# Kernel tuning notes

Measured on AMD Instinct MI355X. Metric: run time of the kernel, lower is better.

## Reference

```python
import jax, jax.numpy as jnp
import numpy as np

B_SZ, L, D_MODEL = 2, 2048, 2048
D_SSM, D_STATE, NHEADS, HEADDIM = 4096, 128, 64, 64
D_CONV, CHUNK = 3, 128
EPS = 1e-5


def setup_inputs() -> dict:
    key = jax.random.key(0)
    k = jax.random.split(key, 8)
    d_in_proj = 2 * D_SSM + 2 * D_STATE + NHEADS  # 8512
    conv_dim = D_SSM + 2 * D_STATE                # 4352
    # dt_bias init exactly as in the torch module (inverse-softplus of dt)
    dt = jnp.exp(jax.random.uniform(k[5], (NHEADS,)) * (np.log(0.1) - np.log(0.001)) + np.log(0.001))
    dt = jnp.clip(dt, 1e-4, None)
    dt_bias = dt + jnp.log(-jnp.expm1(-dt))
    return {
        "u": jax.random.normal(k[0], (B_SZ, L, D_MODEL), jnp.float32),
        "W_in": jax.random.normal(k[1], (d_in_proj, D_MODEL), jnp.float32) * (D_MODEL ** -0.5),
        "conv_w": jax.random.normal(k[2], (conv_dim, D_CONV), jnp.float32) * (D_CONV ** -0.5),
        "conv_b": jnp.zeros((conv_dim,), jnp.float32),
        "dt_bias": dt_bias,
        "A_log": jnp.log(jax.random.uniform(k[3], (NHEADS,), minval=1.0, maxval=16.0)),
        "D": jnp.ones((NHEADS,), jnp.float32),
        "norm_w": jnp.ones((D_SSM,), jnp.float32),
        "W_out": jax.random.normal(k[4], (D_MODEL, D_SSM), jnp.float32) * (D_SSM ** -0.5),
    }


def _silu(x):
    return x * jax.nn.sigmoid(x)


def _segsum(x):
    # x: (..., T) -> (..., T, T) lower-triangular cumulative segment sums; -inf above diag
    T = x.shape[-1]
    cs = jnp.cumsum(x, axis=-1)
    d = cs[..., :, None] - cs[..., None, :]
    mask = jnp.tril(jnp.ones((T, T), dtype=bool))
    return jnp.where(mask, d, -jnp.inf)


def _ssd(X, A, Bm, Cm):
    # Chunked selective-scan (SSD). X (b,l,h,p) is x*dt; A (b,l,h) is dt*A_head (log-decay);
    # Bm, Cm (b,l,n) with ngroups=1.
    nc = L // CHUNK
    X = X.reshape(B_SZ, nc, CHUNK, NHEADS, HEADDIM)
    A = A.reshape(B_SZ, nc, CHUNK, NHEADS).transpose(0, 3, 1, 2)  # (b,h,c,l)
    Bm = Bm.reshape(B_SZ, nc, CHUNK, D_STATE)
    Cm = Cm.reshape(B_SZ, nc, CHUNK, D_STATE)
    A_cum = jnp.cumsum(A, axis=-1)
    Ld = jnp.exp(_segsum(A))  # (b,h,c,l,s) intra-chunk causal decay
    Y_diag = jnp.einsum('bcln,bcsn,bhcls,bcshp->bclhp', Cm, Bm, Ld, X)
    decay_states = jnp.exp(A_cum[..., -1:] - A_cum)  # (b,h,c,l)
    states = jnp.einsum('bcln,bhcl,bclhp->bchpn', Bm, decay_states, X)
    states = jnp.concatenate([jnp.zeros_like(states[:, :1]), states], axis=1)
    decay_chunk = jnp.exp(_segsum(jnp.pad(A_cum[..., -1], ((0, 0), (0, 0), (1, 0)))))  # (b,h,c+1,c+1)
    states = jnp.einsum('bhzc,bchpn->bzhpn', decay_chunk, states)[:, :-1]  # state entering each chunk
    Y_off = jnp.einsum('bcln,bchpn,bhcl->bclhp', Cm, states, jnp.exp(A_cum))
    return (Y_diag + Y_off).reshape(B_SZ, L, NHEADS, HEADDIM)


def reference(u, W_in, conv_w, conv_b, dt_bias, A_log, D, norm_w, W_out):
    zxbcdt = jnp.einsum('bld,ed->ble', u, W_in)  # in_proj (no bias)
    z = zxbcdt[..., :D_SSM]
    xBC = zxbcdt[..., D_SSM:2 * D_SSM + 2 * D_STATE]
    dt = jax.nn.softplus(zxbcdt[..., -NHEADS:] + dt_bias)  # (b,l,h)
    # causal depthwise conv1d + SiLU
    xpad = jnp.pad(xBC, ((0, 0), (D_CONV - 1, 0), (0, 0)))
    xBC = _silu(sum(xpad[:, k:k + L, :] * conv_w[:, k] for k in range(D_CONV)) + conv_b)
    x = xBC[..., :D_SSM].reshape(B_SZ, L, NHEADS, HEADDIM)
    Bm = xBC[..., D_SSM:D_SSM + D_STATE]
    Cm = xBC[..., D_SSM + D_STATE:]
    A = -jnp.exp(A_log)  # (h,)
    y = _ssd(x * dt[..., None], dt * A, Bm, Cm) + D[None, None, :, None] * x
    # gated RMSNorm (norm_before_gate=False: gate first, then normalize)
    y = y.reshape(B_SZ, L, D_SSM) * _silu(z)
    y = y * jax.lax.rsqrt(jnp.mean(y * y, axis=-1, keepdims=True) + EPS) * norm_w
    out = jnp.einsum('ble,de->bld', y, W_out)  # out_proj (no bias)
    return out + out[:, ::-1, :]  # bimamba v0: out + out.flip(seq)
```

## Files before the change

kernel.cpp:

```cpp
#include <hip/hip_runtime.h>

constexpr int B_SZ = 2, LSEQ = 2048, D_MODEL = 2048;
constexpr int D_SSM = 4096, D_STATE = 128, NHEADS = 64, HEADDIM = 64;
constexpr int CHUNK = 128;
constexpr int NCH = LSEQ / CHUNK;
constexpr int BL = B_SZ * LSEQ;
constexpr int DIN = 2 * D_SSM + 2 * D_STATE + NHEADS;
constexpr int DINP = 8576;
constexpr int CONVDIM = D_SSM + 2 * D_STATE;
constexpr int BOFF = D_SSM;
constexpr int COFF = D_SSM + D_STATE;

constexpr size_t OFF_WIN = 0;
constexpr size_t OFF_UB  = OFF_WIN + (size_t)DINP * D_MODEL * 2;
constexpr size_t OFF_ZX  = OFF_UB + (size_t)BL * D_MODEL * 2;
constexpr size_t OFF_XBC = OFF_ZX + (size_t)BL * DINP * 2;
constexpr size_t OFF_DT  = OFF_XBC + (size_t)BL * CONVDIM * 2;
constexpr size_t OFF_ST  = OFF_DT + (size_t)BL * NHEADS * 4;
constexpr size_t OFF_CB  = OFF_ST + (size_t)B_SZ * NCH * NHEADS * HEADDIM * D_STATE * 4;
constexpr size_t OFF_DAS = OFF_CB + (size_t)B_SZ * NCH * CHUNK * CHUNK * 4;
constexpr size_t WS_NEED = OFF_DAS + (size_t)B_SZ * NCH * NHEADS * 4 + 4096;

typedef float f32x4 __attribute__((ext_vector_type(4)));
typedef __bf16 bf16x8 __attribute__((ext_vector_type(8)));

__device__ __forceinline__ unsigned short f2bf(float f) {
  unsigned int x = __float_as_uint(f);
  x += 0x7fffu + ((x >> 16) & 1u);
  return (unsigned short)(x >> 16);
}
__device__ __forceinline__ float bf2f(unsigned short u) {
  return __uint_as_float(((unsigned int)u) << 16);
}

__device__ __forceinline__ void llds16(const unsigned short* g, unsigned short* l) {
  __builtin_amdgcn_global_load_lds(
      (const __attribute__((address_space(1))) unsigned int*)g,
      (__attribute__((address_space(3))) unsigned int*)l, 16, 0, 0);
}

__global__ void k_cvt4(const float4* __restrict__ src, ushort4* __restrict__ dst,
                       int n4, int nsrc4) {
  int i = blockIdx.x * 256 + threadIdx.x;
  if (i >= n4) return;
  float4 v = make_float4(0.f, 0.f, 0.f, 0.f);
  if (i < nsrc4) v = src[i];
  ushort4 o;
  o.x = f2bf(v.x); o.y = f2bf(v.y); o.z = f2bf(v.z); o.w = f2bf(v.w);
  dst[i] = o;
}

template <bool OUT_BF16>
__global__ __launch_bounds__(256, 2) void k_gemm_bt(
    const unsigned short* __restrict__ A, const unsigned short* __restrict__ Bm,
    void* __restrict__ Cv, int M, int N, int K) {
  __shared__ __align__(16) unsigned short As[128 * 32];
  __shared__ __align__(16) unsigned short Bs[128 * 32];
  int t = threadIdx.x;
  int mt = M >> 7, ntl = N >> 7;
  int bid = blockIdx.x;
  int panel = bid / (8 * mt);
  int within = bid - panel * 8 * mt;
  int pw = min(8, ntl - panel * 8);
  int m0 = (within / pw) * 128;
  int n0 = (panel * 8 + within % pw) * 128;
  int w = t >> 6, lane = t & 63;
  int wm = (w >> 1) * 64, wn = (w & 1) * 64;
  int lr = lane & 15;
  f32x4 acc[4][4] = {};
  int sr = t >> 2;
  int swzS = ((sr & 3) ^ ((sr >> 2) & 3));
  int cSrc = ((t & 3) ^ swzS) * 8;
  const unsigned short* Ap = A + (size_t)(m0 + sr) * K + cSrc;
  const unsigned short* Bp = Bm + (size_t)(n0 + sr) * K + cSrc;
  unsigned short* AsW0 = As + w * 512;
  unsigned short* AsW1 = As + 2048 + w * 512;
  unsigned short* BsW0 = Bs + w * 512;
  unsigned short* BsW1 = Bs + 2048 + w * 512;
  int rsel = lane >> 4;
  for (int k0 = 0; k0 < K; k0 += 32) {
    __syncthreads();
    llds16(Ap + k0, AsW0);
    llds16(Ap + (size_t)64 * K + k0, AsW1);
    llds16(Bp + k0, BsW0);
    llds16(Bp + (size_t)64 * K + k0, BsW1);
    __syncthreads();
    bf16x8 af[4], bfv[4];
#pragma unroll
    for (int i = 0; i < 4; i++) {
      int row = wm + i * 16 + lr;
      int slot = rsel ^ ((row & 3) ^ ((row >> 2) & 3));
      af[i] = *(const bf16x8*)&As[row * 32 + slot * 8];
    }
#pragma unroll
    for (int i = 0; i < 4; i++) {
      int row = wn + i * 16 + lr;
      int slot = rsel ^ ((row & 3) ^ ((row >> 2) & 3));
      bfv[i] = *(const bf16x8*)&Bs[row * 32 + slot * 8];
    }
#pragma unroll
    for (int mi = 0; mi < 4; mi++)
#pragma unroll
      for (int ni = 0; ni < 4; ni++)
        acc[mi][ni] = __builtin_amdgcn_mfma_f32_16x16x32_bf16(af[mi], bfv[ni], acc[mi][ni], 0, 0, 0);
  }
  int orow = (lane >> 4) * 4, ocol = lane & 15;
#pragma unroll
  for (int mi = 0; mi < 4; mi++)
#pragma unroll
    for (int ni = 0; ni < 4; ni++) {
      int r0 = m0 + wm + mi * 16 + orow;
      int c0 = n0 + wn + ni * 16 + ocol;
#pragma unroll
      for (int r = 0; r < 4; r++) {
        if (OUT_BF16)
          ((unsigned short*)Cv)[(size_t)(r0 + r) * N + c0] = f2bf(acc[mi][ni][r]);
        else
          ((float*)Cv)[(size_t)(r0 + r) * N + c0] = acc[mi][ni][r];
      }
    }
}

__global__ void k_dt(const unsigned short* __restrict__ zx, const float* __restrict__ dt_bias,
                     float* __restrict__ dt) {
  int id = blockIdx.x * 256 + threadIdx.x;
  int row = id >> 6, h = id & 63;
  float x = bf2f(zx[(size_t)row * DINP + (2 * D_SSM + 2 * D_STATE) + h]) + dt_bias[h];
  dt[id] = (x > 20.f) ? x : log1pf(expf(x));
}

__global__ void k_conv(const unsigned short* __restrict__ zx, const float* __restrict__ cw,
                       const float* __restrict__ cbv, unsigned short* __restrict__ out) {
  int id = blockIdx.x * 256 + threadIdx.x;
  if (id >= BL * CONVDIM) return;
  int c = id % CONVDIM;
  int row = id / CONVDIM;
  int b = row >> 11, l = row & 2047;
  float acc = cbv[c];
#pragma unroll
  for (int k = 0; k < 3; k++) {
    int ls = l + k - 2;
    if (ls >= 0)
      acc += bf2f(zx[(size_t)(b * LSEQ + ls) * DINP + D_SSM + c]) * cw[c * 3 + k];
  }
  out[(size_t)row * CONVDIM + c] = f2bf(acc / (1.f + expf(-acc)));
}

__global__ __launch_bounds__(256) void k_cb(const unsigned short* __restrict__ xBC,
                                            float* __restrict__ cbuf) {
  int bc = blockIdx.x;
  int row0 = bc * CHUNK;
  int t = threadIdx.x;
  __shared__ float Cs[32 * 132];
  int s = t & 127, lh = t >> 7;
  for (int lt = 0; lt < 4; lt++) {
    __syncthreads();
    for (int i = t; i < 32 * 128; i += 256) {
      int l = i >> 7, n = i & 127;
      Cs[l * 132 + n] = bf2f(xBC[(size_t)(row0 + lt * 32 + l) * CONVDIM + COFF + n]);
    }
    __syncthreads();
    float acc[16];
#pragma unroll
    for (int j = 0; j < 16; j++) acc[j] = 0.f;
    const unsigned short* bp = xBC + (size_t)(row0 + s) * CONVDIM + BOFF;
    for (int n4 = 0; n4 < 128; n4 += 4) {
      ushort4 bu = *(const ushort4*)(bp + n4);
      float b0 = bf2f(bu.x), b1 = bf2f(bu.y), b2 = bf2f(bu.z), b3 = bf2f(bu.w);
#pragma unroll
      for (int li = 0; li < 16; li++) {
        float4 cv = *(const float4*)&Cs[(lh * 16 + li) * 132 + n4];
        acc[li] += b0 * cv.x + b1 * cv.y + b2 * cv.z + b3 * cv.w;
      }
    }
#pragma unroll
    for (int li = 0; li < 16; li++) {
      int gl = lt * 32 + lh * 16 + li;
      cbuf[((size_t)bc * 128 + gl) * 128 + s] = acc[li];
    }
  }
}

__global__ __launch_bounds__(256, 2) void k_states(
    const unsigned short* __restrict__ xBC, const float* __restrict__ dt,
    const float* __restrict__ A_log, float* __restrict__ states,
    float* __restrict__ dAsum) {
  constexpr int LP = 136;
  int id = blockIdx.x; int h = id & 63; int bc = id >> 6; int row0 = bc * CHUNK;
  int t = threadIdx.x;
  __shared__ float Acum[128];
  __shared__ float wdec[128];
  __shared__ __align__(16) unsigned short Bt[128 * LP];
  __shared__ __align__(16) unsigned short Xt[64 * LP];
  float Ah = -expf(A_log[h]);
  if (t < 128) Acum[t] = dt[(size_t)(row0 + t) * 64 + h] * Ah;
  __syncthreads();
  for (int off = 1; off < 128; off <<= 1) {
    float v = 0.f;
    bool act = (t < 128) && (t >= off);
    if (act) v = Acum[t - off];
    __syncthreads();
    if (act) Acum[t] += v;
    __syncthreads();
  }
  float Alast = Acum[127];
  if (t < 128) wdec[t] = expf(Alast - Acum[t]);
  if (t == 0) dAsum[id] = Alast;
  __syncthreads();
  for (int i = t; i < 16 * 128; i += 256) {
    int l = i >> 4, n0 = (i & 15) * 8;
    const unsigned short* src = xBC + (size_t)(row0 + l) * CONVDIM + BOFF + n0;
    ushort4 v0 = *(const ushort4*)src;
    ushort4 v1 = *(const ushort4*)(src + 4);
    float wl = wdec[l];
    int ls = l ^ (n0 & 24);
    Bt[(n0 + 0) * LP + ls] = f2bf(bf2f(v0.x) * wl);
    Bt[(n0 + 1) * LP + ls] = f2bf(bf2f(v0.y) * wl);
    Bt[(n0 + 2) * LP + ls] = f2bf(bf2f(v0.z) * wl);
    Bt[(n0 + 3) * LP + ls] = f2bf(bf2f(v0.w) * wl);
    Bt[(n0 + 4) * LP + ls] = f2bf(bf2f(v1.x) * wl);
    Bt[(n0 + 5) * LP + ls] = f2bf(bf2f(v1.y) * wl);
    Bt[(n0 + 6) * LP + ls] = f2bf(bf2f(v1.z) * wl);
    Bt[(n0 + 7) * LP + ls] = f2bf(bf2f(v1.w) * wl);
  }
  for (int i = t; i < 8 * 128; i += 256) {
    int l = i >> 3, p0 = (i & 7) * 8;
    const unsigned short* src = xBC + (size_t)(row0 + l) * CONVDIM + h * HEADDIM + p0;
    ushort4 v0 = *(const ushort4*)src;
    ushort4 v1 = *(const ushort4*)(src + 4);
    float dl = dt[(size_t)(row0 + l) * 64 + h];
    int ls = l ^ (p0 & 24);
    Xt[(p0 + 0) * LP + ls] = f2bf(bf2f(v0.x) * dl);
    Xt[(p0 + 1) * LP + ls] = f2bf(bf2f(v0.y) * dl);
    Xt[(p0 + 2) * LP + ls] = f2bf(bf2f(v0.z) * dl);
    Xt[(p0 + 3) * LP + ls] = f2bf(bf2f(v0.w) * dl);
    Xt[(p0 + 4) * LP + ls] = f2bf(bf2f(v1.x) * dl);
    Xt[(p0 + 5) * LP + ls] = f2bf(bf2f(v1.y) * dl);
    Xt[(p0 + 6) * LP + ls] = f2bf(bf2f(v1.z) * dl);
    Xt[(p0 + 7) * LP + ls] = f2bf(bf2f(v1.w) * dl);
  }
  __syncthreads();
  int w = t >> 6, lane = t & 63;
  int lr = lane & 15, lk = (lane >> 4) * 8;
  int pp = w * 16 + lr;
  f32x4 acc[8] = {};
  for (int k0 = 0; k0 < 128; k0 += 32) {
    bf16x8 af = *(const bf16x8*)&Xt[pp * LP + ((k0 + lk) ^ (pp & 24))];
#pragma unroll
    for (int nt = 0; nt < 8; nt++) {
      int nn = nt * 16 + lr;
      bf16x8 bfr = *(const bf16x8*)&Bt[nn * LP + ((k0 + lk) ^ (nn & 24))];
      acc[nt] = __builtin_amdgcn_mfma_f32_16x16x32_bf16(af, bfr, acc[nt], 0, 0, 0);
    }
  }
  float* sp = states + (size_t)id * 8192;
  int orow = (lane >> 4) * 4, ocol = lane & 15;
#pragma unroll
  for (int nt = 0; nt < 8; nt++)
#pragma unroll
    for (int r = 0; r < 4; r++)
      sp[(w * 16 + orow + r) * 128 + nt * 16 + ocol] = acc[nt][r];
}

__global__ __launch_bounds__(256) void k_scan(float* __restrict__ states,
                                              const float* __restrict__ dAsum) {
  int blk = blockIdx.x;
  int seg = blk & 15, bh = blk >> 4;
  int b = bh >> 6, h = bh & 63;
  int e = seg * 512 + threadIdx.x * 2;
  float cx = 0.f, cy = 0.f;
  for (int c = 0; c < NCH; c++) {
    int bc = b * NCH + c;
    float* p = states + ((size_t)bc * 64 + h) * 8192 + e;
    float dec = expf(dAsum[bc * 64 + h]);
    float2 raw = *(float2*)p;
    float2 cur = {cx, cy};
    *(float2*)p = cur;
    cx = cx * dec + raw.x;
    cy = cy * dec + raw.y;
  }
}

__global__ __launch_bounds__(256, 2) void k_ssd_y(
    const unsigned short* __restrict__ xBC, const float* __restrict__ dt,
    float* __restrict__ states, const float* __restrict__ cbuf,
    const float* __restrict__ A_log, const float* __restrict__ Dv) {
  constexpr int LP = 136;
  int id = blockIdx.x;
  int h = id & 63, bc = id >> 6;
  int row0 = bc * CHUNK;
  int t = threadIdx.x;
  __shared__ float Acum[128];
  __shared__ __align__(16) unsigned short LA[64 * LP];
  __shared__ __align__(16) unsigned short LB[128 * LP];
  float Ah = -expf(A_log[h]);
  if (t < 128) Acum[t] = dt[(size_t)(row0 + t) * 64 + h] * Ah;
  __syncthreads();
  for (int off = 1; off < 128; off <<= 1) {
    float v = 0.f;
    bool act = (t < 128) && (t >= off);
    if (act) v = Acum[t - off];
    __syncthreads();
    if (act) Acum[t] += v;
    __syncthreads();
  }
  float* sp = states + (size_t)id * 8192;
  for (int i4 = t; i4 < 2048; i4 += 256) {
    int p = i4 >> 5, n0 = (i4 & 31) * 4;
    float4 v = *(const float4*)(sp + p * 128 + n0);
    ushort4 o; o.x = f2bf(v.x); o.y = f2bf(v.y); o.z = f2bf(v.z); o.w = f2bf(v.w);
    *(ushort4*)&LA[p * LP + n0] = o;
  }
  for (int i = t; i < 16 * 128; i += 256) {
    int l = i >> 4, n0 = (i & 15) * 8;
    const unsigned short* src = xBC + (size_t)(row0 + l) * CONVDIM + COFF + n0;
    ushort4 v0 = *(const ushort4*)src;
    ushort4 v1 = *(const ushort4*)(src + 4);
    float el = expf(Acum[l]);
    ushort4 o0, o1;
    o0.x = f2bf(bf2f(v0.x) * el); o0.y = f2bf(bf2f(v0.y) * el);
    o0.z = f2bf(bf2f(v0.z) * el); o0.w = f2bf(bf2f(v0.w) * el);
    o1.x = f2bf(bf2f(v1.x) * el); o1.y = f2bf(bf2f(v1.y) * el);
    o1.z = f2bf(bf2f(v1.z) * el); o1.w = f2bf(bf2f(v1.w) * el);
    *(ushort4*)&LB[l * LP + n0] = o0;
    *(ushort4*)&LB[l * LP + n0 + 4] = o1;
  }
  __syncthreads();
  int w = t >> 6, lane = t & 63;
  int lr = lane & 15, lk = (lane >> 4) * 8;
  f32x4 acc[2][4] = {};
#pragma unroll
  for (int k0 = 0; k0 < 128; k0 += 32) {
    bf16x8 af[2], bfv[4];
#pragma unroll
    for (int mt = 0; mt < 2; mt++)
      af[mt] = *(const bf16x8*)&LB[(w * 32 + mt * 16 + lr) * LP + k0 + lk];
#pragma unroll
    for (int nt = 0; nt < 4; nt++)
      bfv[nt] = *(const bf16x8*)&LA[(nt * 16 + lr) * LP + k0 + lk];
#pragma unroll
    for (int mt = 0; mt < 2; mt++)
#pragma unroll
      for (int nt = 0; nt < 4; nt++)
        acc[mt][nt] = __builtin_amdgcn_mfma_f32_16x16x32_bf16(af[mt], bfv[nt], acc[mt][nt], 0, 0, 0);
  }
  __syncthreads();
  for (int i = t; i < 16 * 128; i += 256) {
    int l = i >> 4, s0 = (i & 15) * 8;
    const float* cbp = cbuf + ((size_t)bc * 128 + l) * 128 + s0;
    float4 c0 = *(const float4*)cbp;
    float4 c1 = *(const float4*)(cbp + 4);
    float al = Acum[l];
    ushort4 o0, o1;
    o0.x = (s0 + 0 <= l) ? f2bf(c0.x * expf(al - Acum[s0 + 0])) : 0;
    o0.y = (s0 + 1 <= l) ? f2bf(c0.y * expf(al - Acum[s0 + 1])) : 0;
    o0.z = (s0 + 2 <= l) ? f2bf(c0.z * expf(al - Acum[s0 + 2])) : 0;
    o0.w = (s0 + 3 <= l) ? f2bf(c0.w * expf(al - Acum[s0 + 3])) : 0;
    o1.x = (s0 + 4 <= l) ? f2bf(c1.x * expf(al - Acum[s0 + 4])) : 0;
    o1.y = (s0 + 5 <= l) ? f2bf(c1.y * expf(al - Acum[s0 + 5])) : 0;
    o1.z = (s0 + 6 <= l) ? f2bf(c1.z * expf(al - Acum[s0 + 6])) : 0;
    o1.w = (s0 + 7 <= l) ? f2bf(c1.w * expf(al - Acum[s0 + 7])) : 0;
    *(ushort4*)&LB[l * LP + s0] = o0;
    *(ushort4*)&LB[l * LP + s0 + 4] = o1;
  }
  for (int i = t; i < 8 * 128; i += 256) {
    int s = i >> 3, p0 = (i & 7) * 8;
    const unsigned short* src = xBC + (size_t)(row0 + s) * CONVDIM + h * HEADDIM + p0;
    ushort4 v0 = *(const ushort4*)src;
    ushort4 v1 = *(const ushort4*)(src + 4);
    float dl = dt[(size_t)(row0 + s) * 64 + h];
    int ss = s ^ (p0 & 24);
    LA[(p0 + 0) * LP + ss] = f2bf(bf2f(v0.x) * dl);
    LA[(p0 + 1) * LP + ss] = f2bf(bf2f(v0.y) * dl);
    LA[(p0 + 2) * LP + ss] = f2bf(bf2f(v0.z) * dl);
    LA[(p0 + 3) * LP + ss] = f2bf(bf2f(v0.w) * dl);
    LA[(p0 + 4) * LP + ss] = f2bf(bf2f(v1.x) * dl);
    LA[(p0 + 5) * LP + ss] = f2bf(bf2f(v1.y) * dl);
    LA[(p0 + 6) * LP + ss] = f2bf(bf2f(v1.z) * dl);
    LA[(p0 + 7) * LP + ss] = f2bf(bf2f(v1.w) * dl);
  }
  __syncthreads();
#pragma unroll
  for (int k0 = 0; k0 < 128; k0 += 32) {
    bf16x8 af[2], bfv[4];
#pragma unroll
    for (int mt = 0; mt < 2; mt++)
      af[mt] = *(const bf16x8*)&LB[(w * 32 + mt * 16 + lr) * LP + k0 + lk];
#pragma unroll
    for (int nt = 0; nt < 4; nt++) {
      int pp = nt * 16 + lr;
      bfv[nt] = *(const bf16x8*)&LA[pp * LP + ((k0 + lk) ^ (pp & 24))];
    }
#pragma unroll
    for (int mt = 0; mt < 2; mt++)
#pragma unroll
      for (int nt = 0; nt < 4; nt++)
        acc[mt][nt] = __builtin_amdgcn_mfma_f32_16x16x32_bf16(af[mt], bfv[nt], acc[mt][nt], 0, 0, 0);
  }
  float Dh = Dv[h];
  int orow = (lane >> 4) * 4, ocol = lane & 15;
#pragma unroll
  for (int mt = 0; mt < 2; mt++)
#pragma unroll
    for (int nt = 0; nt < 4; nt++) {
      int l0 = w * 32 + mt * 16 + orow;
      int p = nt * 16 + ocol;
#pragma unroll
      for (int r = 0; r < 4; r++) {
        int l = l0 + r;
        float xv = bf2f(xBC[(size_t)(row0 + l) * CONVDIM + h * HEADDIM + p]);
        sp[l * 64 + p] = acc[mt][nt][r] + Dh * xv;
      }
    }
}

__global__ __launch_bounds__(256) void k_gate_rms(
    const float* __restrict__ Yst, const unsigned short* __restrict__ zx,
    const float* __restrict__ norm_w, unsigned short* __restrict__ ybf) {
  int row = blockIdx.x, t = threadIdx.x;
  int bc = row >> 7, ll = row & 127;
  float vals[16];
  float ss = 0.f;
#pragma unroll
  for (int j = 0; j < 16; j++) {
    int d = t + j * 256;
    int h = d >> 6, p = d & 63;
    float yv = Yst[(((size_t)bc * 64 + h) * 8192) + ll * 64 + p];
    float z = bf2f(zx[(size_t)row * DINP + d]);
    float g = yv * (z / (1.f + expf(-z)));
    vals[j] = g;
    ss += g * g;
  }
#pragma unroll
  for (int off = 32; off > 0; off >>= 1) ss += __shfl_down(ss, off, 64);
  __shared__ float red[4];
  if ((t & 63) == 0) red[t >> 6] = ss;
  __syncthreads();
  float tot = red[0] + red[1] + red[2] + red[3];
  float rms = rsqrtf(tot / (float)D_SSM + 1e-5f);
#pragma unroll
  for (int j = 0; j < 16; j++) {
    int d = t + j * 256;
    ybf[(size_t)row * D_SSM + d] = f2bf(vals[j] * rms * norm_w[d]);
  }
}

__global__ void k_flipadd(float* __restrict__ out) {
  int id = blockIdx.x * 256 + threadIdx.x;
  int d = id & 2047;
  int rem = id >> 11;
  int l = rem & 1023;
  int b = rem >> 10;
  size_t i1 = ((size_t)b * LSEQ + l) * D_MODEL + d;
  size_t i2 = ((size_t)b * LSEQ + (LSEQ - 1 - l)) * D_MODEL + d;
  float a = out[i1], c = out[i2];
  out[i1] = a + c;
  out[i2] = a + c;
}

extern "C" void kernel_launch(void* const* d_in, const int* in_sizes, int n_in,
                              void* d_out, int out_size, void* d_ws, size_t ws_size,
                              hipStream_t stream) {
  if (ws_size < WS_NEED) return;
  const float* u       = (const float*)d_in[0];
  const float* W_in    = (const float*)d_in[1];
  const float* conv_w  = (const float*)d_in[2];
  const float* conv_b  = (const float*)d_in[3];
  const float* dt_bias = (const float*)d_in[4];
  const float* A_log   = (const float*)d_in[5];
  const float* Dv      = (const float*)d_in[6];
  const float* norm_w  = (const float*)d_in[7];
  const float* W_out   = (const float*)d_in[8];
  float* out = (float*)d_out;
  char* ws = (char*)d_ws;

  unsigned short* winb = (unsigned short*)(ws + OFF_WIN);
  unsigned short* ub   = (unsigned short*)(ws + OFF_UB);
  unsigned short* zx   = (unsigned short*)(ws + OFF_ZX);
  unsigned short* xbc  = (unsigned short*)(ws + OFF_XBC);
  float* dtb  = (float*)(ws + OFF_DT);
  float* st   = (float*)(ws + OFF_ST);
  float* cbuf = (float*)(ws + OFF_CB);
  float* dAs  = (float*)(ws + OFF_DAS);

  k_cvt4<<<2097152 / 256, 256, 0, stream>>>((const float4*)u, (ushort4*)ub, 2097152, 2097152);
  k_cvt4<<<4390912 / 256, 256, 0, stream>>>((const float4*)W_in, (ushort4*)winb, 4390912, 4358144);
  k_gemm_bt<true><<<(DINP / 128) * (BL / 128), 256, 0, stream>>>(ub, winb, zx, BL, DINP, D_MODEL);
  k_cvt4<<<2097152 / 256, 256, 0, stream>>>((const float4*)W_out, (ushort4*)ub, 2097152, 2097152);
  k_dt<<<BL * 64 / 256, 256, 0, stream>>>(zx, dt_bias, dtb);
  k_conv<<<(BL * CONVDIM) / 256, 256, 0, stream>>>(zx, conv_w, conv_b, xbc);
  k_cb<<<B_SZ * NCH, 256, 0, stream>>>(xbc, cbuf);
  k_states<<<B_SZ * NCH * NHEADS, 256, 0, stream>>>(xbc, dtb, A_log, st, dAs);
  k_scan<<<B_SZ * NHEADS * 16, 256, 0, stream>>>(st, dAs);
  k_ssd_y<<<B_SZ * NCH * NHEADS, 256, 0, stream>>>(xbc, dtb, st, cbuf, A_log, Dv);
  k_gate_rms<<<BL, 256, 0, stream>>>(st, zx, norm_w, winb);
  k_gemm_bt<false><<<(D_MODEL / 128) * (BL / 128), 256, 0, stream>>>(winb, ub, out, BL, D_MODEL, D_SSM);
  k_flipadd<<<(B_SZ * (LSEQ / 2) * D_MODEL) / 256, 256, 0, stream>>>(out);
}
```

Baseline: 695.2 us.

## Double-buffer GEMM LDS tiles, fuse input casts, vectorize conv, use fast exp

The bf16 GEMM now keeps two LDS tile buffers. The next K-slice is prefetched with global_load_lds while MFMAs run on the current slice, which drops one barrier per iteration and hides load latency. The two fp32-to-bf16 conversion launches for u and W_in are merged into one kernel. The causal conv kernel now handles 8 channels per thread with vector loads and stores. Several expf calls are replaced by __expf, which trades a little accuracy for cheaper transcendentals, and the doubled LDS footprint may affect occupancy.

```diff
diff --git a/kernel.cpp b/kernel.cpp
--- a/kernel.cpp
+++ b/kernel.cpp
@@ -39,6 +39,23 @@
       (__attribute__((address_space(3))) unsigned int*)l, 16, 0, 0);
 }
 
+__global__ void k_cvt_uw(const float4* __restrict__ u, ushort4* __restrict__ ub,
+                         const float4* __restrict__ wi, ushort4* __restrict__ winb) {
+  int i = blockIdx.x * 256 + threadIdx.x;
+  if (i < 2097152) {
+    float4 v = u[i];
+    ushort4 o; o.x = f2bf(v.x); o.y = f2bf(v.y); o.z = f2bf(v.z); o.w = f2bf(v.w);
+    ub[i] = o;
+  } else {
+    int j = i - 2097152;
+    if (j >= 4390912) return;
+    float4 v = make_float4(0.f, 0.f, 0.f, 0.f);
+    if (j < 4358144) v = wi[j];
+    ushort4 o; o.x = f2bf(v.x); o.y = f2bf(v.y); o.z = f2bf(v.z); o.w = f2bf(v.w);
+    winb[j] = o;
+  }
+}
+
 __global__ void k_cvt4(const float4* __restrict__ src, ushort4* __restrict__ dst,
                        int n4, int nsrc4) {
   int i = blockIdx.x * 256 + threadIdx.x;
@@ -54,8 +71,8 @@
 __global__ __launch_bounds__(256, 2) void k_gemm_bt(
     const unsigned short* __restrict__ A, const unsigned short* __restrict__ Bm,
     void* __restrict__ Cv, int M, int N, int K) {
-  __shared__ __align__(16) unsigned short As[128 * 32];
-  __shared__ __align__(16) unsigned short Bs[128 * 32];
+  __shared__ __align__(16) unsigned short As[2][128 * 32];
+  __shared__ __align__(16) unsigned short Bs[2][128 * 32];
   int t = threadIdx.x;
   int mt = M >> 7, ntl = N >> 7;
   int bid = blockIdx.x;
@@ -73,36 +90,42 @@
   int cSrc = ((t & 3) ^ swzS) * 8;
   const unsigned short* Ap = A + (size_t)(m0 + sr) * K + cSrc;
   const unsigned short* Bp = Bm + (size_t)(n0 + sr) * K + cSrc;
-  unsigned short* AsW0 = As + w * 512;
-  unsigned short* AsW1 = As + 2048 + w * 512;
-  unsigned short* BsW0 = Bs + w * 512;
-  unsigned short* BsW1 = Bs + 2048 + w * 512;
+  int wb = w * 512;
+  llds16(Ap, As[0] + wb);
+  llds16(Ap + (size_t)64 * K, As[0] + 2048 + wb);
+  llds16(Bp, Bs[0] + wb);
+  llds16(Bp + (size_t)64 * K, Bs[0] + 2048 + wb);
   int rsel = lane >> 4;
+  int cur = 0;
   for (int k0 = 0; k0 < K; k0 += 32) {
     __syncthreads();
-    llds16(Ap + k0, AsW0);
-    llds16(Ap + (size_t)64 * K + k0, AsW1);
-    llds16(Bp + k0, BsW0);
-    llds16(Bp + (size_t)64 * K + k0, BsW1);
-    __syncthreads();
+    if (k0 + 32 < K) {
+      llds16(Ap + k0 + 32, As[cur ^ 1] + wb);
+      llds16(Ap + (size_t)64 * K + k0 + 32, As[cur ^ 1] + 2048 + wb);
+      llds16(Bp + k0 + 32, Bs[cur ^ 1] + wb);
+      llds16(Bp + (size_t)64 * K + k0 + 32, Bs[cur ^ 1] + 2048 + wb);
+    }
+    const unsigned short* Ac = As[cur];
+    const unsigned short* Bc = Bs[cur];
     bf16x8 af[4], bfv[4];
 #pragma unroll
     for (int i = 0; i < 4; i++) {
       int row = wm + i * 16 + lr;
       int slot = rsel ^ ((row & 3) ^ ((row >> 2) & 3));
-      af[i] = *(const bf16x8*)&As[row * 32 + slot * 8];
+      af[i] = *(const bf16x8*)&Ac[row * 32 + slot * 8];
     }
 #pragma unroll
     for (int i = 0; i < 4; i++) {
       int row = wn + i * 16 + lr;
       int slot = rsel ^ ((row & 3) ^ ((row >> 2) & 3));
-      bfv[i] = *(const bf16x8*)&Bs[row * 32 + slot * 8];
+      bfv[i] = *(const bf16x8*)&Bc[row * 32 + slot * 8];
     }
 #pragma unroll
     for (int mi = 0; mi < 4; mi++)
 #pragma unroll
       for (int ni = 0; ni < 4; ni++)
         acc[mi][ni] = __builtin_amdgcn_mfma_f32_16x16x32_bf16(af[mi], bfv[ni], acc[mi][ni], 0, 0, 0);
+    cur ^= 1;
   }
   int orow = (lane >> 4) * 4, ocol = lane & 15;
 #pragma unroll
@@ -131,19 +154,37 @@
 
 __global__ void k_conv(const unsigned short* __restrict__ zx, const float* __restrict__ cw,
                        const float* __restrict__ cbv, unsigned short* __restrict__ out) {
+  constexpr int C8 = CONVDIM / 8;
   int id = blockIdx.x * 256 + threadIdx.x;
-  if (id >= BL * CONVDIM) return;
-  int c = id % CONVDIM;
-  int row = id / CONVDIM;
+  if (id >= BL * C8) return;
+  int c8 = id % C8;
+  int row = id / C8;
   int b = row >> 11, l = row & 2047;
-  float acc = cbv[c];
+  int c0 = c8 * 8;
+  float acc[8];
+#pragma unroll
+  for (int j = 0; j < 8; j++) acc[j] = cbv[c0 + j];
 #pragma unroll
   for (int k = 0; k < 3; k++) {
     int ls = l + k - 2;
-    if (ls >= 0)
-      acc += bf2f(zx[(size_t)(b * LSEQ + ls) * DINP + D_SSM + c]) * cw[c * 3 + k];
-  }
-  out[(size_t)row * CONVDIM + c] = f2bf(acc / (1.f + expf(-acc)));
+    if (ls < 0) continue;
+    const unsigned short* src = zx + (size_t)(b * LSEQ + ls) * DINP + D_SSM + c0;
+    ushort4 v0 = *(const ushort4*)src;
+    ushort4 v1 = *(const ushort4*)(src + 4);
+    float xv[8] = {bf2f(v0.x), bf2f(v0.y), bf2f(v0.z), bf2f(v0.w),
+                   bf2f(v1.x), bf2f(v1.y), bf2f(v1.z), bf2f(v1.w)};
+#pragma unroll
+    for (int j = 0; j < 8; j++) acc[j] += xv[j] * cw[(c0 + j) * 3 + k];
+  }
+  ushort4 o0, o1;
+  float s[8];
+#pragma unroll
+  for (int j = 0; j < 8; j++) s[j] = acc[j] / (1.f + __expf(-acc[j]));
+  o0.x = f2bf(s[0]); o0.y = f2bf(s[1]); o0.z = f2bf(s[2]); o0.w = f2bf(s[3]);
+  o1.x = f2bf(s[4]); o1.y = f2bf(s[5]); o1.z = f2bf(s[6]); o1.w = f2bf(s[7]);
+  unsigned short* dst = out + (size_t)row * CONVDIM + c0;
+  *(ushort4*)dst = o0;
+  *(ushort4*)(dst + 4) = o1;
 }
 
 __global__ __launch_bounds__(256) void k_cb(const unsigned short* __restrict__ xBC,
@@ -204,7 +245,7 @@
     __syncthreads();
   }
   float Alast = Acum[127];
-  if (t < 128) wdec[t] = expf(Alast - Acum[t]);
+  if (t < 128) wdec[t] = __expf(Alast - Acum[t]);
   if (t == 0) dAsum[id] = Alast;
   __syncthreads();
   for (int i = t; i < 16 * 128; i += 256) {
@@ -272,7 +313,7 @@
   for (int c = 0; c < NCH; c++) {
     int bc = b * NCH + c;
     float* p = states + ((size_t)bc * 64 + h) * 8192 + e;
-    float dec = expf(dAsum[bc * 64 + h]);
+    float dec = __expf(dAsum[bc * 64 + h]);
     float2 raw = *(float2*)p;
     float2 cur = {cx, cy};
     *(float2*)p = cur;
@@ -316,7 +357,7 @@
     const unsigned short* src = xBC + (size_t)(row0 + l) * CONVDIM + COFF + n0;
     ushort4 v0 = *(const ushort4*)src;
     ushort4 v1 = *(const ushort4*)(src + 4);
-    float el = expf(Acum[l]);
+    float el = __expf(Acum[l]);
     ushort4 o0, o1;
     o0.x = f2bf(bf2f(v0.x) * el); o0.y = f2bf(bf2f(v0.y) * el);
     o0.z = f2bf(bf2f(v0.z) * el); o0.w = f2bf(bf2f(v0.w) * el);
@@ -352,14 +393,14 @@
     float4 c1 = *(const float4*)(cbp + 4);
     float al = Acum[l];
     ushort4 o0, o1;
-    o0.x = (s0 + 0 <= l) ? f2bf(c0.x * expf(al - Acum[s0 + 0])) : 0;
-    o0.y = (s0 + 1 <= l) ? f2bf(c0.y * expf(al - Acum[s0 + 1])) : 0;
-    o0.z = (s0 + 2 <= l) ? f2bf(c0.z * expf(al - Acum[s0 + 2])) : 0;
-    o0.w = (s0 + 3 <= l) ? f2bf(c0.w * expf(al - Acum[s0 + 3])) : 0;
-    o1.x = (s0 + 4 <= l) ? f2bf(c1.x * expf(al - Acum[s0 + 4])) : 0;
-    o1.y = (s0 + 5 <= l) ? f2bf(c1.y * expf(al - Acum[s0 + 5])) : 0;
-    o1.z = (s0 + 6 <= l) ? f2bf(c1.z * expf(al - Acum[s0 + 6])) : 0;
-    o1.w = (s0 + 7 <= l) ? f2bf(c1.w * expf(al - Acum[s0 + 7])) : 0;
+    o0.x = (s0 + 0 <= l) ? f2bf(c0.x * __expf(al - Acum[s0 + 0])) : 0;
+    o0.y = (s0 + 1 <= l) ? f2bf(c0.y * __expf(al - Acum[s0 + 1])) : 0;
+    o0.z = (s0 + 2 <= l) ? f2bf(c0.z * __expf(al - Acum[s0 + 2])) : 0;
+    o0.w = (s0 + 3 <= l) ? f2bf(c0.w * __expf(al - Acum[s0 + 3])) : 0;
+    o1.x = (s0 + 4 <= l) ? f2bf(c1.x * __expf(al - Acum[s0 + 4])) : 0;
+    o1.y = (s0 + 5 <= l) ? f2bf(c1.y * __expf(al - Acum[s0 + 5])) : 0;
+    o1.z = (s0 + 6 <= l) ? f2bf(c1.z * __expf(al - Acum[s0 + 6])) : 0;
+    o1.w = (s0 + 7 <= l) ? f2bf(c1.w * __expf(al - Acum[s0 + 7])) : 0;
     *(ushort4*)&LB[l * LP + s0] = o0;
     *(ushort4*)&LB[l * LP + s0 + 4] = o1;
   }
@@ -427,7 +468,7 @@
     int h = d >> 6, p = d & 63;
     float yv = Yst[(((size_t)bc * 64 + h) * 8192) + ll * 64 + p];
     float z = bf2f(zx[(size_t)row * DINP + d]);
-    float g = yv * (z / (1.f + expf(-z)));
+    float g = yv * (z / (1.f + __expf(-z)));
     vals[j] = g;
     ss += g * g;
   }
@@ -483,12 +524,12 @@
   float* cbuf = (float*)(ws + OFF_CB);
   float* dAs  = (float*)(ws + OFF_DAS);
 
-  k_cvt4<<<2097152 / 256, 256, 0, stream>>>((const float4*)u, (ushort4*)ub, 2097152, 2097152);
-  k_cvt4<<<4390912 / 256, 256, 0, stream>>>((const float4*)W_in, (ushort4*)winb, 4390912, 4358144);
+  k_cvt_uw<<<(2097152 + 4390912 + 255) / 256, 256, 0, stream>>>(
+      (const float4*)u, (ushort4*)ub, (const float4*)W_in, (ushort4*)winb);
   k_gemm_bt<true><<<(DINP / 128) * (BL / 128), 256, 0, stream>>>(ub, winb, zx, BL, DINP, D_MODEL);
   k_cvt4<<<2097152 / 256, 256, 0, stream>>>((const float4*)W_out, (ushort4*)ub, 2097152, 2097152);
   k_dt<<<BL * 64 / 256, 256, 0, stream>>>(zx, dt_bias, dtb);
-  k_conv<<<(BL * CONVDIM) / 256, 256, 0, stream>>>(zx, conv_w, conv_b, xbc);
+  k_conv<<<(BL * (CONVDIM / 8)) / 256, 256, 0, stream>>>(zx, conv_w, conv_b, xbc);
   k_cb<<<B_SZ * NCH, 256, 0, stream>>>(xbc, cbuf);
   k_states<<<B_SZ * NCH * NHEADS, 256, 0, stream>>>(xbc, dtb, A_log, st, dAs);
   k_scan<<<B_SZ * NHEADS * 16, 256, 0, stream>>>(st, dAs);
```

New measurement: 737.8 us. 6.1% more time.
